# Optimization experiments

Measured on AMD Instinct MI355X. Metric: run time of the kernel, lower is better.

Reference implementation:

```python
import jax, jax.numpy as jnp
import numpy as np

B, IN, OUT, NC = 4096, 256, 256, 8  # batch, in_dim, out_dim, n_coef


def jacobi_design_matrix(t, alpha, beta, n_coefs):
    """Jacobi polynomials P_0..P_{n-1}(t) via three-term recurrence; t: [..., ]."""
    polys = [jnp.ones_like(t)]
    if n_coefs > 1:
        polys.append((alpha + 1.0) + (alpha + beta + 2.0) * (t - 1.0) * 0.5)
    for n in range(2, n_coefs):
        c = 2.0 * n + alpha + beta
        A = 2.0 * n * (n + alpha + beta) * (c - 2.0)
        Bc = (c - 1.0) * (c * (c - 2.0) * t + alpha * alpha - beta * beta)
        Cc = 2.0 * (n + alpha - 1.0) * (n + beta - 1.0) * c
        polys.append((Bc * polys[-1] - Cc * polys[-2]) / A)
    return jnp.stack(polys, axis=-1)  # [..., n_coefs]


def setup_inputs() -> dict:
    key = jax.random.key(0)
    k1, k2, k3, k4, k5 = jax.random.split(key, 5)
    return {
        "x": jax.random.normal(k1, (B, IN), jnp.float32),
        "coefs": jax.random.normal(k2, (IN, OUT, NC), jnp.float32) * 0.03,
        "alpha_arctanh": jax.random.normal(k3, (), jnp.float32) * 0.1,
        "resid_scale": jax.random.normal(k4, (IN, 1), jnp.float32),
        "spline_scale": jax.random.normal(k5, (IN, OUT), jnp.float32) * 0.1,
    }


def reference(x, coefs, alpha_arctanh, resid_scale, spline_scale):
    alpha = jnp.tanh(alpha_arctanh)
    # spline input map = tanh; design matrix per input element: [B, in, NC]
    dm = jacobi_design_matrix(jnp.tanh(x), alpha, alpha, NC)
    # coefs einsum 'ic,ioc->io' (batched): [B, in, out]
    y = jnp.einsum('bic,ioc->bio', dm, coefs)
    # residual branch (base_act = tanh) + spline scale; dropout is identity (rate 0, deterministic)
    y = resid_scale[None] * jnp.tanh(x)[..., None] + spline_scale[None] * y
    # mean over in_dim -> [B, out]
    return jnp.mean(y, axis=1)
```

## Files before the change

kernel.cpp:

```cpp
#include <hip/hip_runtime.h>
#include <hip/hip_bf16.h>

#define B_SZ 4096
#define IN_D 256
#define OUT_D 256
#define NC 8

#define BM 64
#define BN 32
#define SSTEPS 16
#define TSTRIDE 68

using f32x4 = __attribute__((ext_vector_type(4))) float;
using s16x8 = __attribute__((ext_vector_type(8))) short;

__device__ __forceinline__ unsigned short f2bf(float f) {
    union { float f; unsigned int u; } v; v.f = f;
    return (unsigned short)((v.u + 0x7fffu + ((v.u >> 16) & 1u)) >> 16);
}

__device__ __forceinline__ float fast_tanh(float x) {
    float e = __expf(2.0f * x);
    return 1.0f - 2.0f / (e + 1.0f);
}

__global__ __launch_bounds__(256) void prep_w(
    const float* __restrict__ coefs, const float* __restrict__ alpha_at,
    const float* __restrict__ resid_scale, const float* __restrict__ spline_scale,
    unsigned short* __restrict__ Wg)
{
    const int i = blockIdx.x;
    const int o = threadIdx.x;

    float al = tanhf(alpha_at[0]);
    float mono[NC][NC];
    #pragma unroll
    for (int a = 0; a < NC; a++)
        #pragma unroll
        for (int b = 0; b < NC; b++) mono[a][b] = 0.f;
    mono[0][0] = 1.f;
    mono[1][1] = al + 1.f;
    #pragma unroll
    for (int n = 2; n < NC; n++) {
        float fn = (float)n;
        float c  = 2.f * fn + 2.f * al;
        float An = 2.f * fn * (fn + 2.f * al) * (c - 2.f);
        float Bn = (c - 1.f) * c * (c - 2.f);
        float Cn = 2.f * (fn + al - 1.f) * (fn + al - 1.f) * c;
        #pragma unroll
        for (int j = 0; j < NC; j++) {
            float tm = (j > 0 ? mono[n - 1][j - 1] : 0.f);
            mono[n][j] = (Bn * tm - Cn * mono[n - 2][j]) / An;
        }
    }

    float cf[NC];
    const float* cp = coefs + ((size_t)i * OUT_D + o) * NC;
    #pragma unroll
    for (int c = 0; c < NC; c++) cf[c] = cp[c];
    float ss = spline_scale[i * OUT_D + o];
    float rs = resid_scale[i];

    unsigned short w8[NC];
    #pragma unroll
    for (int j = 0; j < NC; j++) {
        float wv = 0.f;
        #pragma unroll
        for (int c = 0; c < NC; c++) wv += mono[c][j] * cf[c];
        wv *= ss * (1.0f / IN_D);
        if (j == 1) wv += rs * (1.0f / IN_D);
        w8[j] = f2bf(wv);
    }
    uint4 pk;
    unsigned int* pu = (unsigned int*)&pk;
    #pragma unroll
    for (int h = 0; h < 4; h++)
        pu[h] = (unsigned int)w8[2 * h] | ((unsigned int)w8[2 * h + 1] << 16);
    *(uint4*)(Wg + ((size_t)i * OUT_D + o) * NC) = pk;
}

__global__ __launch_bounds__(256) void kan_gemm(
    const float* __restrict__ x, const unsigned short* __restrict__ Wg,
    float* __restrict__ out)
{
    __shared__ __align__(16) float smem[IN_D * TSTRIDE];
    float* lbuf = smem;

    const int tid  = threadIdx.x;
    const int lane = tid & 63;
    const int kg   = tid >> 6;
    const int lr   = lane & 15;
    const int il   = lane >> 4;

    const int bid  = blockIdx.x;
    const int swz  = (bid & 7) * 64 + (bid >> 3);
    const int mblk = swz >> 3, nblk = swz & 7;
    const int bm = mblk * BM, bn = nblk * BN;

    {
        const int i = tid;
        float t[64];
        #pragma unroll
        for (int r = 0; r < 64; r++)
            t[r] = fast_tanh(x[(size_t)(bm + r) * IN_D + i]);
        float* row = smem + i * TSTRIDE;
        #pragma unroll
        for (int k = 0; k < 16; k++) {
            f32x4 w4 = {t[k], t[k + 16], t[k + 32], t[k + 48]};
            *(f32x4*)(row + 4 * k) = w4;
        }
    }
    __syncthreads();

    f32x4 acc[4][2];
    #pragma unroll
    for (int f = 0; f < 4; f++)
        #pragma unroll
        for (int g = 0; g < 2; g++)
            acc[f][g] = (f32x4){0.f, 0.f, 0.f, 0.f};

    #pragma unroll
    for (int s = 0; s < SSTEPS; ++s) {
        const int i0 = kg * 64 + s * 4 + il;

        uint4 bw[2];
        #pragma unroll
        for (int g = 0; g < 2; g++)
            bw[g] = *(const uint4*)(Wg + ((size_t)i0 * OUT_D + bn + g * 16 + lr) * 8);

        f32x4 tv = *(const f32x4*)(smem + i0 * TSTRIDE + lr * 4);

        s16x8 af[4];
        #pragma unroll
        for (int f = 0; f < 4; f++) {
            float t = tv[f];
            float p2 = t * t, p3 = p2 * t, p4 = p3 * t;
            float p5 = p4 * t, p6 = p5 * t, p7 = p6 * t;
            __hip_bfloat162 h0 = __float22bfloat162_rn(make_float2(1.0f, t));
            __hip_bfloat162 h1 = __float22bfloat162_rn(make_float2(p2, p3));
            __hip_bfloat162 h2 = __float22bfloat162_rn(make_float2(p4, p5));
            __hip_bfloat162 h3 = __float22bfloat162_rn(make_float2(p6, p7));
            uint4 pk;
            pk.x = *(unsigned int*)&h0;
            pk.y = *(unsigned int*)&h1;
            pk.z = *(unsigned int*)&h2;
            pk.w = *(unsigned int*)&h3;
            af[f] = *(s16x8*)&pk;
        }

        #pragma unroll
        for (int f = 0; f < 4; f++)
            #pragma unroll
            for (int g = 0; g < 2; g++)
                acc[f][g] = __builtin_amdgcn_mfma_f32_16x16x32_bf16(
                    af[f], *(s16x8*)&bw[g], acc[f][g], 0, 0, 0);
    }

    __syncthreads();
    if (kg > 0) {
        float* dst = &lbuf[(kg - 1) * 64 * 36 + lane * 36];
        #pragma unroll
        for (int f = 0; f < 4; f++)
            #pragma unroll
            for (int g = 0; g < 2; g++)
                *(f32x4*)(dst + f * 8 + g * 4) = acc[f][g];
    }
    __syncthreads();
    if (kg == 0) {
        #pragma unroll
        for (int r = 0; r < 3; r++) {
            const float* src = &lbuf[r * 64 * 36 + lane * 36];
            #pragma unroll
            for (int f = 0; f < 4; f++)
                #pragma unroll
                for (int g = 0; g < 2; g++)
                    acc[f][g] += *(const f32x4*)(src + f * 8 + g * 4);
        }
        #pragma unroll
        for (int f = 0; f < 4; f++)
            #pragma unroll
            for (int g = 0; g < 2; g++)
                #pragma unroll
                for (int j = 0; j < 4; j++) {
                    int r = bm + f * 16 + il * 4 + j;
                    int c = bn + g * 16 + lr;
                    out[(size_t)r * OUT_D + c] = acc[f][g][j];
                }
    }
}

extern "C" void kernel_launch(void* const* d_in, const int* in_sizes, int n_in,
                              void* d_out, int out_size, void* d_ws, size_t ws_size,
                              hipStream_t stream) {
    const float* x     = (const float*)d_in[0];
    const float* coefs = (const float*)d_in[1];
    const float* alpha = (const float*)d_in[2];
    const float* rs    = (const float*)d_in[3];
    const float* ss    = (const float*)d_in[4];
    float* out = (float*)d_out;

    unsigned short* Wg = (unsigned short*)d_ws;

    prep_w<<<dim3(IN_D), dim3(OUT_D), 0, stream>>>(coefs, alpha, rs, ss, Wg);
    kan_gemm<<<dim3((B_SZ / BM) * (OUT_D / BN)), dim3(256), 0, stream>>>(x, Wg, out);
}
```

Measured before the change: 23.64 us.

## Fuse weight prep into GEMM kernel and evaluate Jacobi recurrence per element

After: 26.60 us. +12.6%, slower.

```diff
diff --git a/kernel.cpp b/kernel.cpp
--- a/kernel.cpp
+++ b/kernel.cpp
@@ -6,108 +6,68 @@
 #define OUT_D 256
 #define NC 8
 
-#define BM 64
+#define BM 128
 #define BN 32
 #define SSTEPS 16
-#define TSTRIDE 68
+#define TS 132
 
 using f32x4 = __attribute__((ext_vector_type(4))) float;
 using s16x8 = __attribute__((ext_vector_type(8))) short;
-
-__device__ __forceinline__ unsigned short f2bf(float f) {
-    union { float f; unsigned int u; } v; v.f = f;
-    return (unsigned short)((v.u + 0x7fffu + ((v.u >> 16) & 1u)) >> 16);
-}
 
 __device__ __forceinline__ float fast_tanh(float x) {
     float e = __expf(2.0f * x);
     return 1.0f - 2.0f / (e + 1.0f);
 }
 
-__global__ __launch_bounds__(256) void prep_w(
-    const float* __restrict__ coefs, const float* __restrict__ alpha_at,
-    const float* __restrict__ resid_scale, const float* __restrict__ spline_scale,
-    unsigned short* __restrict__ Wg)
-{
-    const int i = blockIdx.x;
-    const int o = threadIdx.x;
-
-    float al = tanhf(alpha_at[0]);
-    float mono[NC][NC];
-    #pragma unroll
-    for (int a = 0; a < NC; a++)
-        #pragma unroll
-        for (int b = 0; b < NC; b++) mono[a][b] = 0.f;
-    mono[0][0] = 1.f;
-    mono[1][1] = al + 1.f;
-    #pragma unroll
-    for (int n = 2; n < NC; n++) {
-        float fn = (float)n;
-        float c  = 2.f * fn + 2.f * al;
-        float An = 2.f * fn * (fn + 2.f * al) * (c - 2.f);
-        float Bn = (c - 1.f) * c * (c - 2.f);
-        float Cn = 2.f * (fn + al - 1.f) * (fn + al - 1.f) * c;
-        #pragma unroll
-        for (int j = 0; j < NC; j++) {
-            float tm = (j > 0 ? mono[n - 1][j - 1] : 0.f);
-            mono[n][j] = (Bn * tm - Cn * mono[n - 2][j]) / An;
-        }
-    }
-
-    float cf[NC];
-    const float* cp = coefs + ((size_t)i * OUT_D + o) * NC;
-    #pragma unroll
-    for (int c = 0; c < NC; c++) cf[c] = cp[c];
-    float ss = spline_scale[i * OUT_D + o];
-    float rs = resid_scale[i];
-
-    unsigned short w8[NC];
-    #pragma unroll
-    for (int j = 0; j < NC; j++) {
-        float wv = 0.f;
-        #pragma unroll
-        for (int c = 0; c < NC; c++) wv += mono[c][j] * cf[c];
-        wv *= ss * (1.0f / IN_D);
-        if (j == 1) wv += rs * (1.0f / IN_D);
-        w8[j] = f2bf(wv);
-    }
-    uint4 pk;
-    unsigned int* pu = (unsigned int*)&pk;
-    #pragma unroll
-    for (int h = 0; h < 4; h++)
-        pu[h] = (unsigned int)w8[2 * h] | ((unsigned int)w8[2 * h + 1] << 16);
-    *(uint4*)(Wg + ((size_t)i * OUT_D + o) * NC) = pk;
+__device__ __forceinline__ unsigned int pack2(float a, float b) {
+    __hip_bfloat162 h = __float22bfloat162_rn(make_float2(a, b));
+    return *(unsigned int*)&h;
 }
 
-__global__ __launch_bounds__(256) void kan_gemm(
-    const float* __restrict__ x, const unsigned short* __restrict__ Wg,
-    float* __restrict__ out)
+__global__ __launch_bounds__(512) void kan_one(
+    const float* __restrict__ x, const float* __restrict__ coefs,
+    const float* __restrict__ alpha_at, const float* __restrict__ resid_scale,
+    const float* __restrict__ spline_scale, float* __restrict__ out)
 {
-    __shared__ __align__(16) float smem[IN_D * TSTRIDE];
-    float* lbuf = smem;
+    __shared__ __align__(16) float smem[IN_D * TS];
 
     const int tid  = threadIdx.x;
     const int lane = tid & 63;
-    const int kg   = tid >> 6;
+    const int wid  = tid >> 6;
+    const int mh   = wid >> 2;
+    const int kg   = wid & 3;
     const int lr   = lane & 15;
     const int il   = lane >> 4;
 
     const int bid  = blockIdx.x;
-    const int swz  = (bid & 7) * 64 + (bid >> 3);
+    const int swz  = (bid & 7) * 32 + (bid >> 3);
     const int mblk = swz >> 3, nblk = swz & 7;
     const int bm = mblk * BM, bn = nblk * BN;
 
+    const float al = tanhf(alpha_at[0]);
+    const float h  = al + 1.0f;
+    float bc[8], cc[8];
+    bc[0] = bc[1] = cc[0] = cc[1] = 0.f;
+    #pragma unroll
+    for (int n = 2; n < 8; n++) {
+        float fn = (float)n;
+        float c  = 2.f * fn + 2.f * al;
+        float An = 2.f * fn * (fn + 2.f * al) * (c - 2.f);
+        bc[n] = (c - 1.f) * c * (c - 2.f) / An;
+        cc[n] = 2.f * (fn + al - 1.f) * (fn + al - 1.f) * c / An;
+    }
+    const float inv256 = 1.0f / 256.0f;
+    const float r1 = inv256 / h;
+
     {
-        const int i = tid;
-        float t[64];
-        #pragma unroll
-        for (int r = 0; r < 64; r++)
-            t[r] = fast_tanh(x[(size_t)(bm + r) * IN_D + i]);
-        float* row = smem + i * TSTRIDE;
-        #pragma unroll
-        for (int k = 0; k < 16; k++) {
-            f32x4 w4 = {t[k], t[k + 16], t[k + 32], t[k + 48]};
-            *(f32x4*)(row + 4 * k) = w4;
+        const int i  = tid & 255;
+        const int rb = (tid >> 8) * 64;
+        const float* xp = x + (size_t)(bm + rb) * IN_D + i;
+        float* wp = smem + i * TS + rb;
+        #pragma unroll 8
+        for (int k = 0; k < 64; k++) {
+            float t = fast_tanh(xp[(size_t)k * IN_D]);
+            wp[(k & 15) * 4 + (k >> 4)] = t;
         }
     }
     __syncthreads();
@@ -119,46 +79,60 @@
         for (int g = 0; g < 2; g++)
             acc[f][g] = (f32x4){0.f, 0.f, 0.f, 0.f};
 
+    const float* tb = smem + mh * 64 + lr * 4;
+
     #pragma unroll
     for (int s = 0; s < SSTEPS; ++s) {
-        const int i0 = kg * 64 + s * 4 + il;
+        const int i = kg * 64 + s * 4 + il;
 
-        uint4 bw[2];
-        #pragma unroll
-        for (int g = 0; g < 2; g++)
-            bw[g] = *(const uint4*)(Wg + ((size_t)i0 * OUT_D + bn + g * 16 + lr) * 8);
+        const float* cp0 = coefs + ((size_t)i * OUT_D + bn + lr) * NC;
+        f32x4 c0a = *(const f32x4*)(cp0);
+        f32x4 c0b = *(const f32x4*)(cp0 + 4);
+        f32x4 c1a = *(const f32x4*)(cp0 + 16 * NC);
+        f32x4 c1b = *(const f32x4*)(cp0 + 16 * NC + 4);
+        float ss0 = spline_scale[i * OUT_D + bn + lr] * inv256;
+        float ss1 = spline_scale[i * OUT_D + bn + 16 + lr] * inv256;
+        float rsf = resid_scale[i] * r1;
 
-        f32x4 tv = *(const f32x4*)(smem + i0 * TSTRIDE + lr * 4);
+        uint4 b0, b1;
+        b0.x = pack2(ss0 * c0a[0], __builtin_fmaf(ss0, c0a[1], rsf));
+        b0.y = pack2(ss0 * c0a[2], ss0 * c0a[3]);
+        b0.z = pack2(ss0 * c0b[0], ss0 * c0b[1]);
+        b0.w = pack2(ss0 * c0b[2], ss0 * c0b[3]);
+        b1.x = pack2(ss1 * c1a[0], __builtin_fmaf(ss1, c1a[1], rsf));
+        b1.y = pack2(ss1 * c1a[2], ss1 * c1a[3]);
+        b1.z = pack2(ss1 * c1b[0], ss1 * c1b[1]);
+        b1.w = pack2(ss1 * c1b[2], ss1 * c1b[3]);
 
+        f32x4 tv = *(const f32x4*)(tb + (size_t)i * TS);
         s16x8 af[4];
         #pragma unroll
         for (int f = 0; f < 4; f++) {
             float t = tv[f];
-            float p2 = t * t, p3 = p2 * t, p4 = p3 * t;
-            float p5 = p4 * t, p6 = p5 * t, p7 = p6 * t;
-            __hip_bfloat162 h0 = __float22bfloat162_rn(make_float2(1.0f, t));
-            __hip_bfloat162 h1 = __float22bfloat162_rn(make_float2(p2, p3));
-            __hip_bfloat162 h2 = __float22bfloat162_rn(make_float2(p4, p5));
-            __hip_bfloat162 h3 = __float22bfloat162_rn(make_float2(p6, p7));
+            float P[8];
+            P[0] = 1.0f;
+            P[1] = __builtin_fmaf(h, t - 1.0f, h);
+            #pragma unroll
+            for (int n = 2; n < 8; n++)
+                P[n] = __builtin_fmaf(bc[n], t * P[n - 1], -(cc[n] * P[n - 2]));
             uint4 pk;
-            pk.x = *(unsigned int*)&h0;
-            pk.y = *(unsigned int*)&h1;
-            pk.z = *(unsigned int*)&h2;
-            pk.w = *(unsigned int*)&h3;
+            pk.x = pack2(P[0], P[1]);
+            pk.y = pack2(P[2], P[3]);
+            pk.z = pack2(P[4], P[5]);
+            pk.w = pack2(P[6], P[7]);
             af[f] = *(s16x8*)&pk;
         }
 
         #pragma unroll
-        for (int f = 0; f < 4; f++)
-            #pragma unroll
-            for (int g = 0; g < 2; g++)
-                acc[f][g] = __builtin_amdgcn_mfma_f32_16x16x32_bf16(
-                    af[f], *(s16x8*)&bw[g], acc[f][g], 0, 0, 0);
+        for (int f = 0; f < 4; f++) {
+            acc[f][0] = __builtin_amdgcn_mfma_f32_16x16x32_bf16(af[f], *(s16x8*)&b0, acc[f][0], 0, 0, 0);
+            acc[f][1] = __builtin_amdgcn_mfma_f32_16x16x32_bf16(af[f], *(s16x8*)&b1, acc[f][1], 0, 0, 0);
+        }
     }
 
     __syncthreads();
     if (kg > 0) {
-        float* dst = &lbuf[(kg - 1) * 64 * 36 + lane * 36];
+        float* dst = smem + (mh * 3 + kg - 1) * (64 * 36) + lane * 36;
         #pragma unroll
         for (int f = 0; f < 4; f++)
             #pragma unroll
@@ -169,7 +143,7 @@
     if (kg == 0) {
         #pragma unroll
         for (int r = 0; r < 3; r++) {
-            const float* src = &lbuf[r * 64 * 36 + lane * 36];
+            const float* src = smem + (mh * 3 + r) * (64 * 36) + lane * 36;
             #pragma unroll
             for (int f = 0; f < 4; f++)
                 #pragma unroll
@@ -182,7 +156,7 @@
             for (int g = 0; g < 2; g++)
                 #pragma unroll
                 for (int j = 0; j < 4; j++) {
-                    int r = bm + f * 16 + il * 4 + j;
+                    int r = bm + mh * 64 + f * 16 + il * 4 + j;
                     int c = bn + g * 16 + lr;
                     out[(size_t)r * OUT_D + c] = acc[f][g][j];
                 }
@@ -199,8 +173,6 @@
     const float* ss    = (const float*)d_in[4];
     float* out = (float*)d_out;
 
-    unsigned short* Wg = (unsigned short*)d_ws;
-
-    prep_w<<<dim3(IN_D), dim3(OUT_D), 0, stream>>>(coefs, alpha, rs, ss, Wg);
-    kan_gemm<<<dim3((B_SZ / BM) * (OUT_D / BN)), dim3(256), 0, stream>>>(x, Wg, out);
+    kan_one<<<dim3((B_SZ / BM) * (OUT_D / BN)), dim3(512), 0, stream>>>(
+        x, coefs, alpha, rs, ss, out);
 }
```
